# Optimization experiments

Measured on AMD Instinct MI355X. Metric: run time of the kernel, lower is better.

The kernel has to match this reference:

```python
import jax, jax.numpy as jnp
import numpy as np

E, H, I, T = 8, 1024, 2816, 512
E4M3_MAX = 448.0  # torch.finfo(float8_e4m3fn).max


def _quantize_to_fp8(w):
    # per-tensor dynamic scaling, identical to quantize_to_fp8 in the source
    amax = jnp.max(jnp.abs(w))
    scale = jnp.maximum(amax / E4M3_MAX, 1e-12)
    fp8 = (w / scale).astype(jnp.float8_e4m3fn)
    return fp8, scale.reshape(1).astype(jnp.float32)


def setup_inputs() -> dict:
    key = jax.random.key(0)
    k1, k2, k3, k4 = jax.random.split(key, 4)
    x = jax.random.normal(k1, (T, H), jnp.float32)
    expert_idx = jax.random.randint(k2, (T,), 0, E)
    # learned 3D expert params (stored compressed as fp8 + per-tensor scale)
    w_gu = jax.random.normal(k3, (E, 2 * I, H), jnp.float32) * 0.02
    w_d = jax.random.normal(k4, (E, H, I), jnp.float32) * 0.02
    w_gu_fp8, w_gu_scale = _quantize_to_fp8(w_gu)
    w_d_fp8, w_d_scale = _quantize_to_fp8(w_d)
    return {
        "x": x,
        "expert_idx": expert_idx,
        "w_gu_fp8": w_gu_fp8,
        "w_gu_scale": w_gu_scale,
        "w_d_fp8": w_d_fp8,
        "w_d_scale": w_d_scale,
    }


def reference(x, expert_idx, w_gu_fp8, w_gu_scale, w_d_fp8, w_d_scale):
    # materialize(): dequantize fp8 -> high precision (fp8.to(dtype) * scale)
    w_gu = w_gu_fp8.astype(jnp.float32) * w_gu_scale  # [E, 2I, H]
    w_d = w_d_fp8.astype(jnp.float32) * w_d_scale     # [E, H, I]
    # inner experts forward: SwiGLU MLP per expert, top-1 routed tokens
    gu = jnp.einsum('th,efh->tef', x, w_gu)            # [T, E, 2I]
    gate, up = jnp.split(gu, 2, axis=-1)               # [T, E, I] each
    h = jax.nn.silu(gate) * up                          # [T, E, I]
    y = jnp.einsum('tei,ehi->teh', h, w_d)              # [T, E, H]
    out = y[jnp.arange(x.shape[0]), expert_idx]         # [T, H] select routed expert
    return out
```

## Files before the change

kernel.cpp:

```cpp
#include <hip/hip_runtime.h>
#include <hip/hip_bf16.h>
#include <stdint.h>

#define E_ 8
#define H_ 1024
#define I_ 2816
#define T_ 512

typedef __attribute__((ext_vector_type(4))) float f32x4;
typedef __attribute__((ext_vector_type(8))) short short8;

typedef __attribute__((address_space(1))) const unsigned GAS;
typedef __attribute__((address_space(3))) unsigned LAS;

__device__ __forceinline__ void dma16(const void* g, void* l) {
    __builtin_amdgcn_global_load_lds((GAS*)g, (LAS*)l, 16, 0, 0);
}
__device__ __forceinline__ unsigned short f2bf(float f) {
    return __builtin_bit_cast(unsigned short, __float2bfloat16(f));
}
__device__ __forceinline__ uint32_t pack_rne(float lo, float hi) {
    return (uint32_t)f2bf(lo) | ((uint32_t)f2bf(hi) << 16);
}
__device__ __forceinline__ uint32_t pack_trunc(float lo, float hi) {
    return (__builtin_bit_cast(uint32_t, hi) & 0xFFFF0000u) |
           (__builtin_bit_cast(uint32_t, lo) >> 16);
}

#define SB()  __builtin_amdgcn_sched_barrier(0)
#define VM6() asm volatile("s_waitcnt vmcnt(6)" ::: "memory")
#define VM0() asm volatile("s_waitcnt vmcnt(0)" ::: "memory")

__global__ __launch_bounds__(256) void route_cvt(const float* __restrict__ x,
                                                 const int* __restrict__ idx,
                                                 int* __restrict__ counts,
                                                 int* __restrict__ bucket,
                                                 unsigned short* __restrict__ xg) {
    int tid = threadIdx.x;
    if (blockIdx.x == 0) {
        if (tid < E_) counts[tid] = 0;
        for (int i = tid; i < E_ * T_; i += 256) bucket[i] = 0;
        __syncthreads();
#pragma unroll
        for (int k = 0; k < 2; ++k) {
            int t = tid + k * 256;
            int e = idx[t];
            int pos = atomicAdd(counts + e, 1);
            bucket[e * T_ + pos] = t;
        }
    }
    int unit = blockIdx.x * 256 + tid;
    const float* xp = x + (size_t)unit * 8;
    float4 a = *(const float4*)xp, b = *(const float4*)(xp + 4);
    uint4 o = make_uint4(pack_rne(a.x, a.y), pack_rne(a.z, a.w),
                         pack_rne(b.x, b.y), pack_rne(b.z, b.w));
    *(uint4*)(xg + (size_t)unit * 8) = o;
}

__global__ __launch_bounds__(256, 2) void gemm1(const unsigned short* __restrict__ xg,
                                                const float* __restrict__ wgu,
                                                const float* __restrict__ sgu_p,
                                                const int* __restrict__ counts,
                                                const int* __restrict__ bucket,
                                                __hip_bfloat16* __restrict__ hbuf) {
    int e = blockIdx.x;
    int f0 = blockIdx.y * 8;
    int cnt = counts[e];

    __shared__ __align__(16) char smem[64 * 1024 + 512];
    int* tok = (int*)(smem + 64 * 1024);
    int tid = threadIdx.x, w = tid >> 6, lane = tid & 63;
    int r16 = lane & 15, kg = lane >> 4;

    if (tid < 128) tok[tid] = bucket[e * T_ + tid];
    SB();

    const char* gbase = (const char*)wgu + ((size_t)e * 2 * I_ + f0) * H_ * 4;
    const char* ubase = (const char*)wgu + ((size_t)e * 2 * I_ + I_ + f0) * H_ * 4;
    int soff = w * 1024 + lane * 16;

#define P1SRC(c) ((((c) < 8) ? (gbase + (size_t)(c) * 4096) : (ubase + (size_t)((c) - 8) * 4096)) + soff)
#pragma unroll
    for (int c = 0; c < 16; ++c) dma16(P1SRC(c), smem + c * 4096 + soff);
    SB();

#define P1(c, n)                                                              \
    do {                                                                      \
        asm volatile("s_waitcnt vmcnt(" #n ")" ::: "memory"); SB();           \
        float4 v = *(const float4*)(smem + (c) * 4096 + tid * 16);            \
        SB();                                                                 \
        __builtin_amdgcn_s_barrier();                                         \
        uint2 o; o.x = pack_trunc(v.x, v.y); o.y = pack_trunc(v.z, v.w);      \
        *(uint2*)(smem + (c) * 2048 + (((tid >> 1) ^ ((c) & 7)) * 16) + (tid & 1) * 8) = o; \
    } while (0)

    P1(0, 15);  P1(1, 14);  P1(2, 13);  P1(3, 12);
    P1(4, 11);  P1(5, 10);  P1(6, 9);   P1(7, 8);
    P1(8, 7);   P1(9, 6);   P1(10, 5);  P1(11, 4);
    P1(12, 3);  P1(13, 2);  P1(14, 1);  P1(15, 0);
#undef P1
#undef P1SRC
    __syncthreads();

    const char* a0p = (const char*)xg + (size_t)tok[w * 32 + r16] * 2048 + kg * 16;
    const char* a1p = (const char*)xg + (size_t)tok[w * 32 + 16 + r16] * 2048 + kg * 16;

    f32x4 acc[2];
    acc[0] = (f32x4){0, 0, 0, 0};
    acc[1] = (f32x4){0, 0, 0, 0};

#pragma unroll 4
    for (int t = 0; t < 16; ++t) {
#pragma unroll
        for (int kk = 0; kk < 2; ++kk) {
            short8 Bf = *(const short8*)(smem + r16 * 2048 +
                         (((t * 8 + kk * 4 + kg) ^ (r16 & 7)) * 16));
            short8 A0 = *(const short8*)(a0p + t * 128 + kk * 64);
            short8 A1 = *(const short8*)(a1p + t * 128 + kk * 64);
            acc[0] = __builtin_amdgcn_mfma_f32_16x16x32_bf16(A0, Bf, acc[0], 0, 0, 0);
            acc[1] = __builtin_amdgcn_mfma_f32_16x16x32_bf16(A1, Bf, acc[1], 0, 0, 0);
        }
    }

    float sgu = sgu_p[0];
#pragma unroll
    for (int m = 0; m < 2; ++m)
#pragma unroll
        for (int j = 0; j < 4; ++j) {
            float self = acc[m][j] * sgu;
            float other = __shfl_xor(self, 8);
            if (r16 < 8) {
                float g = self, u = other;
                float hv = (g / (1.f + __expf(-g))) * u;
                int tk = w * 32 + m * 16 + kg * 4 + j;
                if (tk < cnt)
                    hbuf[(size_t)tok[tk] * I_ + f0 + r16] = __float2bfloat16(hv);
            }
        }
}

__global__ __launch_bounds__(256) void gemm2(const __hip_bfloat16* __restrict__ hbuf,
                                             const float* __restrict__ wd,
                                             const float* __restrict__ sd_p,
                                             const int* __restrict__ counts,
                                             const int* __restrict__ bucket,
                                             float* __restrict__ out) {
    int e = blockIdx.x >> 1, mt = blockIdx.x & 1;
    int cnt = counts[e];
    if (mt * 64 >= cnt) return;
    int h0 = blockIdx.y * 16;

    __shared__ __align__(16) char smem[72 * 1024 + 256];
    int* tok = (int*)(smem + 72 * 1024);
    int tid = threadIdx.x, w = tid >> 6, lane = tid & 63;
    int r16 = lane & 15, kg = lane >> 4;

    float sd = sd_p[0];
    asm volatile("" :: "v"(sd));

    if (tid < 64) tok[tid] = bucket[e * T_ + mt * 64 + tid];
    __syncthreads();

    const char* hb = (const char*)hbuf;
    const char* srcA[4]; char* dstA[4];
#pragma unroll
    for (int i = 0; i < 4; ++i) {
        int U = (w * 4 + i) * 64 + lane;
        int row = U >> 4, sl = U & 15;
        srcA[i] = hb + (size_t)tok[row] * (I_ * 2) + (size_t)((sl ^ (row & 15)) * 16);
        dstA[i] = smem + (w * 4 + i) * 1024;
    }
    const char* wd_e = (const char*)(wd + (size_t)e * (size_t)H_ * I_);
    const char* srcB[2]; char* dstB[2];
#pragma unroll
    for (int i = 0; i < 2; ++i) {
        int U = (w * 2 + i) * 64 + lane;
        int row = U >> 5, sl = U & 31;
        srcB[i] = wd_e + (size_t)(h0 + row) * ((size_t)I_ * 4) + (size_t)((sl ^ (row & 15)) * 16);
        dstB[i] = smem + 48 * 1024 + (w * 2 + i) * 1024;
    }

#define G2_ISSUE(s, buf)                                                     \
    do {                                                                     \
        _Pragma("unroll")                                                    \
        for (int i = 0; i < 4; ++i) dma16(srcA[i] + (size_t)(s) * 256, dstA[i] + (buf) * 16384); \
        _Pragma("unroll")                                                    \
        for (int i = 0; i < 2; ++i) dma16(srcB[i] + (size_t)(s) * 512, dstB[i] + (buf) * 8192);  \
    } while (0)

    G2_ISSUE(0, 0);
    G2_ISSUE(1, 1);

    f32x4 acc = (f32x4){0, 0, 0, 0};

    for (int t = 0; t < 22; ++t) {
        VM6();
        __builtin_amdgcn_s_barrier();
        int tp = (t + 2 < 22) ? t + 2 : 21;
        G2_ISSUE(tp, (t + 2) % 3);
        const char* Ab = smem + (t % 3) * 16384;
        const char* Bb = smem + 48 * 1024 + (t % 3) * 8192;
#pragma unroll
        for (int kk = 0; kk < 4; ++kk) {
            int bo = r16 * 512 + kk * 128 + kg * 32;
            int sw = r16 << 4;
            float4 b0 = *(float4*)(Bb + (bo ^ sw));
            float4 b1 = *(float4*)(Bb + ((bo + 16) ^ sw));
            uint4 bu = make_uint4(pack_trunc(b0.x, b0.y), pack_trunc(b0.z, b0.w),
                                  pack_trunc(b1.x, b1.y), pack_trunc(b1.z, b1.w));
            short8 B = __builtin_bit_cast(short8, bu);
            int ar = w * 16 + r16;
            short8 A = *(short8*)(Ab + ((ar * 256 + kk * 64 + kg * 16) ^ ((ar & 15) << 4)));
            acc = __builtin_amdgcn_mfma_f32_16x16x32_bf16(A, B, acc, 0, 0, 0);
        }
    }
    VM0();

#pragma unroll
    for (int j = 0; j < 4; ++j) {
        int tr = w * 16 + kg * 4 + j;
        int pos = mt * 64 + tr;
        if (pos < cnt)
            out[(size_t)tok[tr] * H_ + h0 + r16] = acc[j] * sd;
    }
#undef G2_ISSUE
}

extern "C" void kernel_launch(void* const* d_in, const int* in_sizes, int n_in,
                              void* d_out, int out_size, void* d_ws, size_t ws_size,
                              hipStream_t stream) {
    const float* x    = (const float*)d_in[0];
    const int*   eidx = (const int*)d_in[1];
    const float* wgu  = (const float*)d_in[2];
    const float* sgu  = (const float*)d_in[3];
    const float* wd   = (const float*)d_in[4];
    const float* sd   = (const float*)d_in[5];
    float* out = (float*)d_out;

    char* ws = (char*)d_ws;
    int* counts = (int*)ws;
    int* bucket = (int*)(ws + 1024);
    unsigned short* xg = (unsigned short*)(ws + 32768);
    __hip_bfloat16* hbuf = (__hip_bfloat16*)(ws + 1114112);

    route_cvt<<<256, 256, 0, stream>>>(x, eidx, counts, bucket, xg);
    gemm1<<<dim3(E_, I_ / 8), 256, 0, stream>>>(xg, wgu, sgu, counts, bucket, hbuf);
    gemm2<<<dim3(E_ * 2, H_ / 16), 256, 0, stream>>>(hbuf, wd, sd, counts, bucket, out);
}
```

Before: 140.8 us.

## Stage gathered token activations through an LDS ring buffer with async DMA prefetch

The gate/up GEMM used to read the gathered x rows straight from global memory into registers for every MFMA. It now copies them with global_load_lds into a four-slot LDS ring, keeps three K-steps of DMA in flight and waits on vmcnt before each step. The aim is to hide global gather latency behind the MFMAs and use a swizzled LDS layout for the A fragments. In exchange it costs more LDS, a fully serialized 32-step loop with a sched barrier, and redundant tail loads to keep the wait counts consistent.

```diff
diff --git a/kernel.cpp b/kernel.cpp
--- a/kernel.cpp
+++ b/kernel.cpp
@@ -29,6 +29,7 @@
 
 #define SB()  __builtin_amdgcn_sched_barrier(0)
 #define VM6() asm volatile("s_waitcnt vmcnt(6)" ::: "memory")
+#define VM4() asm volatile("s_waitcnt vmcnt(4)" ::: "memory")
 #define VM0() asm volatile("s_waitcnt vmcnt(0)" ::: "memory")
 
 __global__ __launch_bounds__(256) void route_cvt(const float* __restrict__ x,
@@ -102,24 +103,41 @@
 #undef P1SRC
     __syncthreads();
 
-    const char* a0p = (const char*)xg + (size_t)tok[w * 32 + r16] * 2048 + kg * 16;
-    const char* a1p = (const char*)xg + (size_t)tok[w * 32 + 16 + r16] * 2048 + kg * 16;
+    const char* xb = (const char*)xg;
+    const char* srcA[2]; char* dstA[2];
+#pragma unroll
+    for (int i = 0; i < 2; ++i) {
+        int U = (w * 2 + i) * 64 + lane;
+        int row = U >> 2, sl = U & 3;
+        srcA[i] = xb + (size_t)tok[row] * 2048 + ((sl ^ (row & 3)) * 16);
+        dstA[i] = smem + 32 * 1024 + (w * 2 + i) * 1024;
+    }
+#pragma unroll
+    for (int b = 0; b < 3; ++b)
+#pragma unroll
+        for (int i = 0; i < 2; ++i)
+            dma16(srcA[i] + (size_t)b * 64, dstA[i] + b * 8192);
 
     f32x4 acc[2];
     acc[0] = (f32x4){0, 0, 0, 0};
     acc[1] = (f32x4){0, 0, 0, 0};
 
-#pragma unroll 4
-    for (int t = 0; t < 16; ++t) {
-#pragma unroll
-        for (int kk = 0; kk < 2; ++kk) {
-            short8 Bf = *(const short8*)(smem + r16 * 2048 +
-                         (((t * 8 + kk * 4 + kg) ^ (r16 & 7)) * 16));
-            short8 A0 = *(const short8*)(a0p + t * 128 + kk * 64);
-            short8 A1 = *(const short8*)(a1p + t * 128 + kk * 64);
-            acc[0] = __builtin_amdgcn_mfma_f32_16x16x32_bf16(A0, Bf, acc[0], 0, 0, 0);
-            acc[1] = __builtin_amdgcn_mfma_f32_16x16x32_bf16(A1, Bf, acc[1], 0, 0, 0);
-        }
+    for (int t = 0; t < 32; ++t) {
+        VM4();
+        SB();
+        const char* Ab = smem + 32 * 1024 + (t & 3) * 8192;
+        short8 Bf = *(const short8*)(smem + r16 * 2048 +
+                     (((t * 4 + kg) ^ (r16 & 7)) * 16));
+#pragma unroll
+        for (int m = 0; m < 2; ++m) {
+            int tr = w * 32 + m * 16 + r16;
+            short8 Af = *(const short8*)(Ab + tr * 64 + ((kg ^ (tr & 3)) * 16));
+            acc[m] = __builtin_amdgcn_mfma_f32_16x16x32_bf16(Af, Bf, acc[m], 0, 0, 0);
+        }
+        int tp = (t + 3 < 32) ? t + 3 : 31;
+#pragma unroll
+        for (int i = 0; i < 2; ++i)
+            dma16(srcA[i] + (size_t)tp * 64, dstA[i] + ((t + 3) & 3) * 8192);
     }
 
     float sgu = sgu_p[0];
```

After: 118.3 us. 16.0% less time.
